# Performance work log

Hardware: AMD Instinct MI355X
Metric: run time of the kernel (lower is better)

Reference implementation:

```python
import jax, jax.numpy as jnp
import numpy as np

B, S, D, H, HID, WIN = 2, 2048, 1024, 16, 4096, 256
DH = D // H
HALF = WIN // 2  # symmetric half-window


def _layernorm(x, w, b, eps=1e-5):
    mu = jnp.mean(x, axis=-1, keepdims=True)
    var = jnp.var(x, axis=-1, keepdims=True)
    return (x - mu) * jax.lax.rsqrt(var + eps) * w + b


def setup_inputs() -> dict:
    key = jax.random.key(0)
    ks = jax.random.split(key, 8)
    std = 0.02
    return {
        "x": jax.random.normal(ks[0], (B, S, D), jnp.float32),
        "mask": jnp.ones((B, S), bool),
        "ln1_w": jnp.ones((D,), jnp.float32),
        "ln1_b": jnp.zeros((D,), jnp.float32),
        "Wq": jax.random.normal(ks[1], (D, D), jnp.float32) * std,
        "bq": jnp.zeros((D,), jnp.float32),
        "Wk": jax.random.normal(ks[2], (D, D), jnp.float32) * std,
        "bk": jnp.zeros((D,), jnp.float32),
        "Wv": jax.random.normal(ks[3], (D, D), jnp.float32) * std,
        "bv": jnp.zeros((D,), jnp.float32),
        "Wo": jax.random.normal(ks[4], (D, D), jnp.float32) * std,
        "bo": jnp.zeros((D,), jnp.float32),
        "ln2_w": jnp.ones((D,), jnp.float32),
        "ln2_b": jnp.zeros((D,), jnp.float32),
        "Wg": jax.random.normal(ks[5], (D, HID), jnp.float32) * std,
        "bg": jnp.zeros((HID,), jnp.float32),
        "Wu": jax.random.normal(ks[6], (D, HID), jnp.float32) * std,
        "bu": jnp.zeros((HID,), jnp.float32),
        "Wd": jax.random.normal(ks[7], (HID, D), jnp.float32) * std,
        "bd": jnp.zeros((D,), jnp.float32),
    }


def reference(x, mask, ln1_w, ln1_b, Wq, bq, Wk, bk, Wv, bv, Wo, bo,
              ln2_w, ln2_b, Wg, bg, Wu, bu, Wd, bd):
    # ---- pre-norm windowed self-attention ----
    h = _layernorm(x, ln1_w, ln1_b)
    q = (h @ Wq + bq).reshape(B, S, H, DH)
    k = (h @ Wk + bk).reshape(B, S, H, DH)
    v = (h @ Wv + bv).reshape(B, S, H, DH)
    scores = jnp.einsum('bshd,bthd->bhst', q, k) / jnp.sqrt(jnp.float32(DH))
    idx = jnp.arange(S)
    band = jnp.abs(idx[:, None] - idx[None, :]) <= HALF          # [S,S] sliding window
    allow = band[None, None, :, :] & mask[:, None, None, :]      # band AND key padding
    scores = jnp.where(allow, scores, jnp.float32(-1e9))
    attn = jax.nn.softmax(scores, axis=-1)
    ctx = jnp.einsum('bhst,bthd->bshd', attn, v).reshape(B, S, D)
    x = x + (ctx @ Wo + bo)
    # ---- pre-norm SwiGLU FFN ----
    h2 = _layernorm(x, ln2_w, ln2_b)
    ffn = (jax.nn.silu(h2 @ Wg + bg) * (h2 @ Wu + bu)) @ Wd + bd
    return x + ffn
```

## Files before the change

### kernel.cpp

```cpp
#include <hip/hip_runtime.h>
#include <stdint.h>


typedef __bf16 bf16;
typedef bf16  bf16x8 __attribute__((ext_vector_type(8)));
typedef bf16  bf16x4v __attribute__((ext_vector_type(4)));
typedef float f32x4  __attribute__((ext_vector_type(4)));

#define S_LEN 2048

#define GLDS16(gp, lp)                                                          \
  __builtin_amdgcn_global_load_lds(                                            \
      (__attribute__((address_space(1))) void*)(gp),                            \
      (__attribute__((address_space(3))) void*)(lp), 16, 0, 0)

__global__ __launch_bounds__(256) void ln_bf16(const float* __restrict__ x,
                                               const float* __restrict__ w,
                                               const float* __restrict__ bb,
                                               bf16* __restrict__ out) {
  const int row = blockIdx.x, tid = threadIdx.x;
  const int wid = tid >> 6, lane = tid & 63;
  const float4 v = ((const float4*)(x + (size_t)row * 1024))[tid];
  float s = v.x + v.y + v.z + v.w;
  float q = v.x * v.x + v.y * v.y + v.z * v.z + v.w * v.w;
#pragma unroll
  for (int off = 32; off > 0; off >>= 1) {
    s += __shfl_xor(s, off);
    q += __shfl_xor(q, off);
  }
  __shared__ float rs_[4], rq_[4];
  if (lane == 0) { rs_[wid] = s; rq_[wid] = q; }
  __syncthreads();
  s = rs_[0] + rs_[1] + rs_[2] + rs_[3];
  q = rq_[0] + rq_[1] + rq_[2] + rq_[3];
  const float mean = s * (1.f / 1024.f);
  const float var  = q * (1.f / 1024.f) - mean * mean;
  const float rstd = rsqrtf(var + 1e-5f);
  const float4 wv = ((const float4*)w)[tid];
  const float4 bv = ((const float4*)bb)[tid];
  bf16x4v o;
  o[0] = (bf16)((v.x - mean) * rstd * wv.x + bv.x);
  o[1] = (bf16)((v.y - mean) * rstd * wv.y + bv.y);
  o[2] = (bf16)((v.z - mean) * rstd * wv.z + bv.z);
  o[3] = (bf16)((v.w - mean) * rstd * wv.w + bv.w);
  ((bf16x4v*)(out + (size_t)row * 1024))[tid] = o;
}

__global__ __launch_bounds__(256) void tr_cast(const float* __restrict__ in,
                                               bf16* __restrict__ out, int R, int C) {
  __shared__ float t[32][33];
  const int tx = threadIdx.x, ty = threadIdx.y;
  const int r0 = blockIdx.y * 32, c0 = blockIdx.x * 32;
#pragma unroll
  for (int i = 0; i < 4; ++i)
    t[ty + 8 * i][tx] = in[(size_t)(r0 + ty + 8 * i) * C + c0 + tx];
  __syncthreads();
#pragma unroll
  for (int i = 0; i < 4; ++i)
    out[(size_t)(c0 + ty + 8 * i) * R + r0 + tx] = (bf16)t[tx][ty + 8 * i];
}

__global__ void concat3(const float* __restrict__ a, const float* __restrict__ b,
                        const float* __restrict__ c, float* __restrict__ o) {
  int i = blockIdx.x * 256 + threadIdx.x;
  if (i < 1024) o[i] = a[i];
  else if (i < 2048) o[i] = b[i - 1024];
  else if (i < 3072) o[i] = c[i - 2048];
}

#define PHASE8(p, a, b, STG, VM)                                               \
  {                                                                            \
    STG;                                                                       \
    if ((VM) == 10) asm volatile("s_waitcnt vmcnt(10)" ::: "memory");          \
    __builtin_amdgcn_s_barrier();                                              \
    const char* sA_ = smA + ((p) << 15) + ((a) << 14);                         \
    const char* sB_ = smB + ((p) << 15) + ((b) << 14);                         \
    bf16x8 av[4][2], bv[2][2];                                                 \
    _Pragma("unroll") for (int q = 0; q < 4; ++q) {                            \
      av[q][0] = *(const bf16x8*)(sA_ + aRow + q * 2048 + kh0);                \
      av[q][1] = *(const bf16x8*)(sA_ + aRow + q * 2048 + kh1);                \
    }                                                                          \
    _Pragma("unroll") for (int n_ = 0; n_ < 2; ++n_) {                         \
      bv[n_][0] = *(const bf16x8*)(sB_ + bRow + n_ * 2048 + kh0);              \
      bv[n_][1] = *(const bf16x8*)(sB_ + bRow + n_ * 2048 + kh1);              \
    }                                                                          \
    __builtin_amdgcn_s_setprio(1);                                             \
    _Pragma("unroll") for (int q = 0; q < 4; ++q)                              \
      _Pragma("unroll") for (int n_ = 0; n_ < 2; ++n_) {                       \
        acc[(a)*4 + q][(b)*2 + n_] = __builtin_amdgcn_mfma_f32_16x16x32_bf16(  \
            av[q][0], bv[n_][0], acc[(a)*4 + q][(b)*2 + n_], 0, 0, 0);         \
        acc[(a)*4 + q][(b)*2 + n_] = __builtin_amdgcn_mfma_f32_16x16x32_bf16(  \
            av[q][1], bv[n_][1], acc[(a)*4 + q][(b)*2 + n_], 0, 0, 0);         \
      }                                                                        \
    __builtin_amdgcn_s_setprio(0);                                             \
    __builtin_amdgcn_s_barrier();                                              \
  }

template <int EPI>
__global__ __launch_bounds__(512, 2) void gemm256p(
    const bf16* __restrict__ A, const bf16* __restrict__ BT,
    const bf16* __restrict__ BT2, const float* __restrict__ bias,
    const float* __restrict__ bias2, bf16* __restrict__ outp,
    bf16* __restrict__ vout, bf16* __restrict__ pout,
    int Astr, int Bstr) {
  __shared__ char smem[131072];
  char* smA = smem;
  char* smB = smem + 65536;

  const int tid = threadIdx.x, wid = tid >> 6, lane = tid & 63;
  const int fr = lane & 15, fq = lane >> 4;
  const int wr = wid >> 2, wc = wid & 3;
  const int wm = wr * 128, wn = wc * 64;

  int wg = blockIdx.x;
  {
    const int nwg = gridDim.x;
    int qq = nwg >> 3, rr = nwg & 7, xc = wg & 7, ix = wg >> 3;
    wg = (xc < rr ? xc * (qq + 1) : rr * (qq + 1) + (xc - rr) * qq) + ix;
  }
  int mtile, ntile, ks = 0;
  if constexpr (EPI == 3) { mtile = wg & 15; ntile = (wg >> 4) & 3; ks = wg >> 6; }
  else                    { mtile = wg & 15; ntile = wg >> 4; }
  const int m0 = mtile * 256;
  const int nbase = (EPI == 2) ? ntile * 128 : ntile * 256;
  const size_t kbase = (size_t)ks << 10;

  const int lr = tid >> 3;
  const int segS = ((tid & 7) ^ (lr & 7)) * 8;
  const bf16* pAc0a0 = A + (size_t)(m0 + lr) * Astr + kbase + segS;
  const bf16* pAc0a1 = A + (size_t)(m0 + 64 + lr) * Astr + kbase + segS;
  const bf16* pAc1a0 = A + (size_t)(m0 + 128 + lr) * Astr + kbase + segS;
  const bf16* pAc1a1 = A + (size_t)(m0 + 192 + lr) * Astr + kbase + segS;
  const int nn0 = (lr >> 5) * 64 + (lr & 31);
  const bf16 *pBc0b0, *pBc0b1, *pBc1b0, *pBc1b1;
  if constexpr (EPI == 2) {
    pBc0b0 = BT  + (size_t)(nbase + nn0) * Bstr + kbase + segS;
    pBc0b1 = BT  + (size_t)(nbase + nn0 + 32) * Bstr + kbase + segS;
    pBc1b0 = BT2 + (size_t)(nbase + nn0) * Bstr + kbase + segS;
    pBc1b1 = BT2 + (size_t)(nbase + nn0 + 32) * Bstr + kbase + segS;
  } else {
    pBc0b0 = BT + (size_t)(nbase + nn0) * Bstr + kbase + segS;
    pBc0b1 = BT + (size_t)(nbase + nn0 + 32) * Bstr + kbase + segS;
    pBc1b0 = BT + (size_t)(nbase + 128 + nn0) * Bstr + kbase + segS;
    pBc1b1 = BT + (size_t)(nbase + 128 + nn0 + 32) * Bstr + kbase + segS;
  }
  const int widOff = wid * 1024;

  auto stA = [&](int p, int a, int kt) {
    const size_t ko = (size_t)kt * 64;
    char* d = smA + (p << 15) + (a << 14) + widOff;
    GLDS16((a ? pAc0a1 : pAc0a0) + ko, d);
    GLDS16((a ? pAc1a1 : pAc1a0) + ko, d + 8192);
  };
  auto stB = [&](int p, int b, int kt) {
    const size_t ko = (size_t)kt * 64;
    char* d = smB + (p << 15) + (b << 14) + widOff;
    GLDS16((b ? pBc0b1 : pBc0b0) + ko, d);
    GLDS16((b ? pBc1b1 : pBc1b0) + ko, d + 8192);
  };

  const int co0 = (fq * 16) ^ ((fr & 3) << 4);
  const int kh0 = (fr & 4) << 4;
  const int kh1 = 64 ^ kh0;
  const int aRow = (wr * 64 + fr) * 128 + co0;
  const int bRow = (wc * 32 + fr) * 128 + co0;

  f32x4 acc[8][4];
#pragma unroll
  for (int i = 0; i < 8; ++i)
#pragma unroll
    for (int j = 0; j < 4; ++j) acc[i][j] = f32x4{0.f, 0.f, 0.f, 0.f};

  stB(0, 0, 0); stA(0, 0, 0); stA(0, 1, 0); stB(0, 1, 0);
  stB(1, 0, 1); stA(1, 0, 1);

  for (int t2 = 0; t2 < 8; ++t2) {
    const int te = 2 * t2, to = te + 1;
    PHASE8(0, 0, 0, stA(1, 1, (te + 1) & 15), 10)
    PHASE8(0, 1, 0, stB(1, 1, (te + 1) & 15), 10)
    PHASE8(0, 0, 1, stB(0, 0, (te + 2) & 15), 10)
    PHASE8(0, 1, 1, stA(0, 0, (te + 2) & 15), -1)
    PHASE8(1, 0, 0, stA(0, 1, (to + 1) & 15), 10)
    PHASE8(1, 1, 0, stB(0, 1, (to + 1) & 15), 10)
    PHASE8(1, 0, 1, stB(1, 0, (to + 2) & 15), 10)
    PHASE8(1, 1, 1, stA(1, 0, (to + 2) & 15), -1)
  }
  asm volatile("s_waitcnt vmcnt(0)" ::: "memory");
  __builtin_amdgcn_s_barrier();

  if constexpr (EPI == 1) {
    if (nbase < 2048) {
#pragma unroll
      for (int mi = 0; mi < 8; ++mi)
#pragma unroll
        for (int nj = 0; nj < 4; ++nj) {
          const int grow = m0 + wm + mi * 16 + fq * 4;
          const int gcol = nbase + wn + nj * 16 + fr;
          const float bc = bias[gcol];
#pragma unroll
          for (int r = 0; r < 4; ++r)
            outp[(size_t)(grow + r) * 2048 + gcol] = (bf16)(acc[mi][nj][r] + bc);
        }
    } else {
#pragma unroll
      for (int mi = 0; mi < 8; ++mi)
#pragma unroll
        for (int nj = 0; nj < 4; ++nj) {
          const int grow = m0 + wm + mi * 16 + fq * 4;
          const int gcol = nbase + wn + nj * 16 + fr;
          const float bc = bias[gcol];
          bf16x4v pk;
#pragma unroll
          for (int r = 0; r < 4; ++r) pk[r] = (bf16)(acc[mi][nj][r] + bc);
          *(bf16x4v*)(vout + ((size_t)((grow >> 11) * 1024 + (gcol - 2048))) * 2048 +
                      (grow & 2047)) = pk;
        }
    }
  } else if constexpr (EPI == 2) {
    float* uls = (float*)smem;
    if (wn >= 128) {
#pragma unroll
      for (int mi = 0; mi < 8; ++mi)
#pragma unroll
        for (int nj = 0; nj < 4; ++nj) {
          const int rowL = wm + mi * 16 + fq * 4;
          const int cu = wn - 128 + nj * 16 + fr;
          const float bc = bias2[nbase + cu];
#pragma unroll
          for (int r = 0; r < 4; ++r)
            uls[(rowL + r) * 128 + cu] = acc[mi][nj][r] + bc;
        }
    }
    __syncthreads();
    if (wn < 128) {
#pragma unroll
      for (int mi = 0; mi < 8; ++mi)
#pragma unroll
        for (int nj = 0; nj < 4; ++nj) {
          const int rowL = wm + mi * 16 + fq * 4;
          const int cg = wn + nj * 16 + fr;
          const float bc = bias[nbase + cg];
#pragma unroll
          for (int r = 0; r < 4; ++r) {
            const float g = acc[mi][nj][r] + bc;
            const float u = uls[(rowL + r) * 128 + cg];
            outp[(size_t)(m0 + rowL + r) * 4096 + nbase + cg] =
                (bf16)(g * u / (1.f + __expf(-g)));
          }
        }
    }
  } else {
    bf16* po = pout + ((size_t)ks << 22);
#pragma unroll
    for (int mi = 0; mi < 8; ++mi)
#pragma unroll
      for (int nj = 0; nj < 4; ++nj) {
        const int grow = m0 + wm + mi * 16 + fq * 4;
        const int gcol = nbase + wn + nj * 16 + fr;
#pragma unroll
        for (int r = 0; r < 4; ++r)
          po[(size_t)(grow + r) * 1024 + gcol] = (bf16)acc[mi][nj][r];
      }
  }
}

__global__ __launch_bounds__(256) void reduce_wd(
    const float* __restrict__ x1, const float* __restrict__ bd,
    const bf16* __restrict__ parts, float* __restrict__ out) {
  const size_t i = (size_t)blockIdx.x * 256 + threadIdx.x;
  const float4 a  = ((const float4*)x1)[i];
  const float4 bv = ((const float4*)bd)[i & 255];
  float s0 = a.x + bv.x, s1 = a.y + bv.y, s2 = a.z + bv.z, s3 = a.w + bv.w;
#pragma unroll
  for (int k = 0; k < 4; ++k) {
    const bf16x4v p = ((const bf16x4v*)(parts + ((size_t)k << 22)))[i];
    s0 += (float)p[0]; s1 += (float)p[1]; s2 += (float)p[2]; s3 += (float)p[3];
  }
  ((float4*)out)[i] = make_float4(s0, s1, s2, s3);
}

template <int EPI>
__global__ __launch_bounds__(256) void gemm_bf16t(
    const bf16* __restrict__ A, const bf16* __restrict__ BT,
    const float* __restrict__ bias, const float* __restrict__ res,
    void* __restrict__ Cout, int M, int N, int K) {
  __shared__ bf16 sA[128 * 64];
  __shared__ bf16 sB[128 * 64];
  const int tid = threadIdx.x;
  const int wid = tid >> 6, lane = tid & 63;
  const int m0 = blockIdx.y * 128, n0 = blockIdx.x * 128;
  const int wm = (wid >> 1) * 64, wn = (wid & 1) * 64;
  const int lrow = lane >> 3, lseg = (lane & 7) * 8;
  const int fr = lane & 15, fq = lane >> 4;

  f32x4 acc[4][4];
#pragma unroll
  for (int i = 0; i < 4; ++i)
#pragma unroll
    for (int j = 0; j < 4; ++j) acc[i][j] = f32x4{0.f, 0.f, 0.f, 0.f};

  for (int k0 = 0; k0 < K; k0 += 64) {
#pragma unroll
    for (int it = 0; it < 4; ++it) {
      const int c = wid * 4 + it;
      const int row = c * 8 + lrow;
      GLDS16(A  + (size_t)(m0 + row) * K + k0 + lseg, sA + c * 512);
      GLDS16(BT + (size_t)(n0 + row) * K + k0 + lseg, sB + c * 512);
    }
    __syncthreads();
#pragma unroll
    for (int kk = 0; kk < 64; kk += 32) {
      bf16x8 af[4], bfv[4];
#pragma unroll
      for (int i = 0; i < 4; ++i)
        af[i] = *(const bf16x8*)(sA + (wm + i * 16 + fr) * 64 + kk + 8 * fq);
#pragma unroll
      for (int j = 0; j < 4; ++j)
        bfv[j] = *(const bf16x8*)(sB + (wn + j * 16 + fr) * 64 + kk + 8 * fq);
#pragma unroll
      for (int i = 0; i < 4; ++i)
#pragma unroll
        for (int j = 0; j < 4; ++j)
          acc[i][j] = __builtin_amdgcn_mfma_f32_16x16x32_bf16(af[i], bfv[j],
                                                              acc[i][j], 0, 0, 0);
    }
    __syncthreads();
  }

#pragma unroll
  for (int i = 0; i < 4; ++i) {
    const int grow = m0 + wm + i * 16 + fq * 4;
#pragma unroll
    for (int j = 0; j < 4; ++j) {
      const int gcol = n0 + wn + j * 16 + fr;
      const float bc = bias[gcol];
#pragma unroll
      for (int r = 0; r < 4; ++r) {
        const size_t idx = (size_t)(grow + r) * N + gcol;
        const float v = acc[i][j][r] + bc;
        if constexpr (EPI == 1) {
          ((float*)Cout)[idx] = v + res[idx];
        } else {
          ((bf16*)Cout)[idx] = (bf16)v;
        }
      }
    }
  }
}

__global__ __launch_bounds__(256) void attn_mfma(const bf16* __restrict__ qk,
                                                 const bf16* __restrict__ vT,
                                                 bf16* __restrict__ ctx) {
  __shared__ bf16 sQ[64 * 72];
  __shared__ bf16 sK[320 * 72];
  __shared__ bf16 sVT[64 * 328];
  __shared__ bf16 sP[64 * 328];
  const int bh = blockIdx.x;
  const int b = bh >> 4, h = bh & 15;
  const int qs0 = blockIdx.y * 64;
  const int t0 = qs0 - 128;
  const int tS = t0 < 0 ? 0 : (t0 > S_LEN - 320 ? S_LEN - 320 : t0);
  const int tid = threadIdx.x, wid = tid >> 6, lane = tid & 63;
  const size_t bbase = (size_t)b * S_LEN;

#pragma unroll
  for (int i = 0; i < 10; ++i) {
    const int c = i * 256 + tid, row = c >> 3, seg = (c & 7) * 8;
    *(bf16x8*)(sK + row * 72 + seg) =
        *(const bf16x8*)(qk + (bbase + tS + row) * 2048 + 1024 + h * 64 + seg);
  }
#pragma unroll
  for (int i = 0; i < 2; ++i) {
    const int c = i * 256 + tid, row = c >> 3, seg = (c & 7) * 8;
    *(bf16x8*)(sQ + row * 72 + seg) =
        *(const bf16x8*)(qk + (bbase + qs0 + row) * 2048 + h * 64 + seg);
  }
  {
    const int row = tid >> 2;
    const size_t vbase = ((size_t)bh * 64 + row) * 2048 + tS;
#pragma unroll
    for (int i = 0; i < 10; ++i) {
      const int seg = ((tid & 3) + 4 * i) * 8;
      *(bf16x8*)(sVT + row * 328 + seg) = *(const bf16x8*)(vT + vbase + seg);
    }
  }
  __syncthreads();

  const int fr = lane & 15, fq = lane >> 4;

  f32x4 s[20];
#pragma unroll
  for (int j = 0; j < 20; ++j) s[j] = f32x4{0.f, 0.f, 0.f, 0.f};
#pragma unroll
  for (int kk = 0; kk < 64; kk += 32) {
    const bf16x8 aq = *(const bf16x8*)(sQ + (wid * 16 + fr) * 72 + kk + 8 * fq);
#pragma unroll
    for (int j = 0; j < 20; ++j) {
      const bf16x8 bk = *(const bf16x8*)(sK + (j * 16 + fr) * 72 + kk + 8 * fq);
      s[j] = __builtin_amdgcn_mfma_f32_16x16x32_bf16(aq, bk, s[j], 0, 0, 0);
    }
  }

#pragma unroll
  for (int r = 0; r < 4; ++r) {
    const int q_g = qs0 + wid * 16 + fq * 4 + r;
    float m = -1e30f;
#pragma unroll
    for (int j = 0; j < 20; ++j) {
      const int t_g = tS + j * 16 + fr;
      const bool ok = (unsigned)(q_g - t_g + 128) <= 256u;
      const float val = ok ? s[j][r] * 0.125f : -1e30f;
      s[j][r] = val;
      m = fmaxf(m, val);
    }
#pragma unroll
    for (int off = 1; off < 16; off <<= 1) m = fmaxf(m, __shfl_xor(m, off));
    float sm = 0.f;
#pragma unroll
    for (int j = 0; j < 20; ++j) {
      const float p = __expf(s[j][r] - m);
      s[j][r] = p;
      sm += p;
    }
#pragma unroll
    for (int off = 1; off < 16; off <<= 1) sm += __shfl_xor(sm, off);
    const float inv = 1.f / sm;
#pragma unroll
    for (int j = 0; j < 20; ++j)
      sP[(wid * 16 + fq * 4 + r) * 328 + j * 16 + fr] = (bf16)(s[j][r] * inv);
  }
  __syncthreads();

  f32x4 o[4];
#pragma unroll
  for (int j = 0; j < 4; ++j) o[j] = f32x4{0.f, 0.f, 0.f, 0.f};
#pragma unroll
  for (int ks = 0; ks < 10; ++ks) {
    const int kk = ks * 32;
    const bf16x8 pa = *(const bf16x8*)(sP + (wid * 16 + fr) * 328 + kk + 8 * fq);
#pragma unroll
    for (int j = 0; j < 4; ++j) {
      const bf16x8 vb = *(const bf16x8*)(sVT + (j * 16 + fr) * 328 + kk + 8 * fq);
      o[j] = __builtin_amdgcn_mfma_f32_16x16x32_bf16(pa, vb, o[j], 0, 0, 0);
    }
  }
#pragma unroll
  for (int j = 0; j < 4; ++j)
#pragma unroll
    for (int r = 0; r < 4; ++r) {
      const int q = qs0 + wid * 16 + fq * 4 + r;
      ctx[(bbase + q) * 1024 + h * 64 + j * 16 + fr] = (bf16)o[j][r];
    }
}

extern "C" void kernel_launch(void* const* d_in, const int* in_sizes, int n_in,
                              void* d_out, int out_size, void* d_ws, size_t ws_size,
                              hipStream_t stream) {
  const float* x    = (const float*)d_in[0];
  const float* ln1w = (const float*)d_in[2];
  const float* ln1b = (const float*)d_in[3];
  const float* Wq   = (const float*)d_in[4];
  const float* bq   = (const float*)d_in[5];
  const float* Wk   = (const float*)d_in[6];
  const float* bk   = (const float*)d_in[7];
  const float* Wv   = (const float*)d_in[8];
  const float* bv   = (const float*)d_in[9];
  const float* Wo   = (const float*)d_in[10];
  const float* bo   = (const float*)d_in[11];
  const float* ln2w = (const float*)d_in[12];
  const float* ln2b = (const float*)d_in[13];
  const float* Wg   = (const float*)d_in[14];
  const float* bg   = (const float*)d_in[15];
  const float* Wu   = (const float*)d_in[16];
  const float* bu   = (const float*)d_in[17];
  const float* Wd   = (const float*)d_in[18];
  const float* bd   = (const float*)d_in[19];

  char* ws = (char*)d_ws;
  size_t off = 0;
  auto take = [&](size_t bytes) {
    char* p = ws + off;
    off += (bytes + 255) & ~(size_t)255;
    return p;
  };
  bf16*  wqkvT = (bf16*)take((size_t)3072 * 1024 * 2);
  bf16*  woT   = (bf16*)take((size_t)1024 * 1024 * 2);
  bf16*  wgT   = (bf16*)take((size_t)4096 * 1024 * 2);
  bf16*  wuT   = (bf16*)take((size_t)4096 * 1024 * 2);
  bf16*  wdT   = (bf16*)take((size_t)1024 * 4096 * 2);
  float* bqkv  = (float*)take((size_t)3072 * 4);
  bf16*  h     = (bf16*)take((size_t)4096 * 1024 * 2);
  bf16*  qk    = (bf16*)take((size_t)4096 * 2048 * 2);
  bf16*  ctx   = (bf16*)take((size_t)4096 * 1024 * 2);
  bf16*  vT    = (bf16*)take((size_t)2048 * 2048 * 2);
  float* x1    = (float*)take((size_t)4096 * 1024 * 4);
  bf16*  h2    = (bf16*)take((size_t)4096 * 1024 * 2);
  bf16*  gated = (bf16*)take((size_t)4096 * 4096 * 2);
  bf16*  parts = h;
  (void)ws_size; (void)in_sizes; (void)n_in; (void)out_size;

  const dim3 tb(32, 8);
  tr_cast<<<dim3(32, 32), tb, 0, stream>>>(Wq, wqkvT, 1024, 1024);
  tr_cast<<<dim3(32, 32), tb, 0, stream>>>(Wk, wqkvT + (size_t)1024 * 1024, 1024, 1024);
  tr_cast<<<dim3(32, 32), tb, 0, stream>>>(Wv, wqkvT + (size_t)2048 * 1024, 1024, 1024);
  tr_cast<<<dim3(32, 32), tb, 0, stream>>>(Wo, woT, 1024, 1024);
  tr_cast<<<dim3(128, 32), tb, 0, stream>>>(Wg, wgT, 1024, 4096);
  tr_cast<<<dim3(128, 32), tb, 0, stream>>>(Wu, wuT, 1024, 4096);
  tr_cast<<<dim3(32, 128), tb, 0, stream>>>(Wd, wdT, 4096, 1024);
  concat3<<<12, 256, 0, stream>>>(bq, bk, bv, bqkv);

  ln_bf16<<<4096, 256, 0, stream>>>(x, ln1w, ln1b, h);
  gemm256p<1><<<192, 512, 0, stream>>>(h, wqkvT, nullptr, bqkv, nullptr,
                                       qk, vT, nullptr, 1024, 1024);
  attn_mfma<<<dim3(32, 32), 256, 0, stream>>>(qk, vT, ctx);
  gemm_bf16t<1><<<dim3(8, 32), 256, 0, stream>>>(ctx, woT, bo, x,
                                                 x1, 4096, 1024, 1024);
  ln_bf16<<<4096, 256, 0, stream>>>(x1, ln2w, ln2b, h2);
  gemm256p<2><<<512, 512, 0, stream>>>(h2, wgT, wuT, bg, bu, gated,
                                       nullptr, nullptr, 1024, 1024);
  gemm256p<3><<<256, 512, 0, stream>>>(gated, wdT, nullptr, nullptr, nullptr,
                                       nullptr, nullptr, parts, 4096, 4096);
  reduce_wd<<<4096, 256, 0, stream>>>(x1, bd, parts, (float*)d_out);
}
```

Baseline: 265.8 us.

## Replace 8-phase GEMM pipeline with simple double-buffered stage/compute loop

Replaces the fine-grained 8-phase interleaved staging schedule (quarter-tile loads and barriers per phase) with a plain two-buffer ping-pong. Each full k-tile of A and B is loaded into one buffer while the other is computed. Each wave now loads a contiguous 32-row slab, and each warp covers its whole 128x64 output per compute step, reusing B fragments across two A halves. This cuts barrier count and scheduling complexity, but gives coarser overlap of global loads with MFMA work.

```diff
diff --git a/kernel.cpp b/kernel.cpp
--- a/kernel.cpp
+++ b/kernel.cpp
@@ -68,34 +68,6 @@
   else if (i < 3072) o[i] = c[i - 2048];
 }
 
-#define PHASE8(p, a, b, STG, VM)                                               \
-  {                                                                            \
-    STG;                                                                       \
-    if ((VM) == 10) asm volatile("s_waitcnt vmcnt(10)" ::: "memory");          \
-    __builtin_amdgcn_s_barrier();                                              \
-    const char* sA_ = smA + ((p) << 15) + ((a) << 14);                         \
-    const char* sB_ = smB + ((p) << 15) + ((b) << 14);                         \
-    bf16x8 av[4][2], bv[2][2];                                                 \
-    _Pragma("unroll") for (int q = 0; q < 4; ++q) {                            \
-      av[q][0] = *(const bf16x8*)(sA_ + aRow + q * 2048 + kh0);                \
-      av[q][1] = *(const bf16x8*)(sA_ + aRow + q * 2048 + kh1);                \
-    }                                                                          \
-    _Pragma("unroll") for (int n_ = 0; n_ < 2; ++n_) {                         \
-      bv[n_][0] = *(const bf16x8*)(sB_ + bRow + n_ * 2048 + kh0);              \
-      bv[n_][1] = *(const bf16x8*)(sB_ + bRow + n_ * 2048 + kh1);              \
-    }                                                                          \
-    __builtin_amdgcn_s_setprio(1);                                             \
-    _Pragma("unroll") for (int q = 0; q < 4; ++q)                              \
-      _Pragma("unroll") for (int n_ = 0; n_ < 2; ++n_) {                       \
-        acc[(a)*4 + q][(b)*2 + n_] = __builtin_amdgcn_mfma_f32_16x16x32_bf16(  \
-            av[q][0], bv[n_][0], acc[(a)*4 + q][(b)*2 + n_], 0, 0, 0);         \
-        acc[(a)*4 + q][(b)*2 + n_] = __builtin_amdgcn_mfma_f32_16x16x32_bf16(  \
-            av[q][1], bv[n_][1], acc[(a)*4 + q][(b)*2 + n_], 0, 0, 0);         \
-      }                                                                        \
-    __builtin_amdgcn_s_setprio(0);                                             \
-    __builtin_amdgcn_s_barrier();                                              \
-  }
-
 template <int EPI>
 __global__ __launch_bounds__(512, 2) void gemm256p(
     const bf16* __restrict__ A, const bf16* __restrict__ BT,
@@ -104,8 +76,10 @@
     bf16* __restrict__ vout, bf16* __restrict__ pout,
     int Astr, int Bstr) {
   __shared__ char smem[131072];
-  char* smA = smem;
-  char* smB = smem + 65536;
+  char* A0 = smem;
+  char* A1 = smem + 32768;
+  char* B0 = smem + 65536;
+  char* B1 = smem + 98304;
 
   const int tid = threadIdx.x, wid = tid >> 6, lane = tid & 63;
   const int fr = lane & 15, fq = lane >> 4;
@@ -125,45 +99,34 @@
   const int nbase = (EPI == 2) ? ntile * 128 : ntile * 256;
   const size_t kbase = (size_t)ks << 10;
 
-  const int lr = tid >> 3;
-  const int segS = ((tid & 7) ^ (lr & 7)) * 8;
-  const bf16* pAc0a0 = A + (size_t)(m0 + lr) * Astr + kbase + segS;
-  const bf16* pAc0a1 = A + (size_t)(m0 + 64 + lr) * Astr + kbase + segS;
-  const bf16* pAc1a0 = A + (size_t)(m0 + 128 + lr) * Astr + kbase + segS;
-  const bf16* pAc1a1 = A + (size_t)(m0 + 192 + lr) * Astr + kbase + segS;
-  const int nn0 = (lr >> 5) * 64 + (lr & 31);
-  const bf16 *pBc0b0, *pBc0b1, *pBc1b0, *pBc1b1;
+  const int srow = lane >> 3;
+  const int segS = ((lane & 7) ^ srow) * 8;
+  const size_t rsA8 = (size_t)8 * Astr;
+  const size_t rsB8 = (size_t)8 * Bstr;
+  const bf16* pA = A + (size_t)(m0 + wid * 32 + srow) * Astr + kbase + segS;
+  const bf16* pB;
   if constexpr (EPI == 2) {
-    pBc0b0 = BT  + (size_t)(nbase + nn0) * Bstr + kbase + segS;
-    pBc0b1 = BT  + (size_t)(nbase + nn0 + 32) * Bstr + kbase + segS;
-    pBc1b0 = BT2 + (size_t)(nbase + nn0) * Bstr + kbase + segS;
-    pBc1b1 = BT2 + (size_t)(nbase + nn0 + 32) * Bstr + kbase + segS;
+    const bf16* srcB = (wid < 4) ? BT : BT2;
+    pB = srcB + (size_t)(nbase + (wid & 3) * 32 + srow) * Bstr + kbase + segS;
   } else {
-    pBc0b0 = BT + (size_t)(nbase + nn0) * Bstr + kbase + segS;
-    pBc0b1 = BT + (size_t)(nbase + nn0 + 32) * Bstr + kbase + segS;
-    pBc1b0 = BT + (size_t)(nbase + 128 + nn0) * Bstr + kbase + segS;
-    pBc1b1 = BT + (size_t)(nbase + 128 + nn0 + 32) * Bstr + kbase + segS;
-  }
-  const int widOff = wid * 1024;
-
-  auto stA = [&](int p, int a, int kt) {
+    pB = BT + (size_t)(nbase + wid * 32 + srow) * Bstr + kbase + segS;
+  }
+  const int cOff = wid * 4096;
+
+  auto STAGE = [&](char* aD, char* bD, int kt) {
     const size_t ko = (size_t)kt * 64;
-    char* d = smA + (p << 15) + (a << 14) + widOff;
-    GLDS16((a ? pAc0a1 : pAc0a0) + ko, d);
-    GLDS16((a ? pAc1a1 : pAc1a0) + ko, d + 8192);
-  };
-  auto stB = [&](int p, int b, int kt) {
-    const size_t ko = (size_t)kt * 64;
-    char* d = smB + (p << 15) + (b << 14) + widOff;
-    GLDS16((b ? pBc0b1 : pBc0b0) + ko, d);
-    GLDS16((b ? pBc1b1 : pBc1b0) + ko, d + 8192);
+#pragma unroll
+    for (int i = 0; i < 4; ++i) {
+      GLDS16(pA + i * rsA8 + ko, aD + cOff + i * 1024);
+      GLDS16(pB + i * rsB8 + ko, bD + cOff + i * 1024);
+    }
   };
 
   const int co0 = (fq * 16) ^ ((fr & 3) << 4);
   const int kh0 = (fr & 4) << 4;
   const int kh1 = 64 ^ kh0;
-  const int aRow = (wr * 64 + fr) * 128 + co0;
-  const int bRow = (wc * 32 + fr) * 128 + co0;
+  const int aOff = (wm + fr) * 128 + co0;
+  const int bOff = (wn + fr) * 128 + co0;
 
   f32x4 acc[8][4];
 #pragma unroll
@@ -171,22 +134,55 @@
 #pragma unroll
     for (int j = 0; j < 4; ++j) acc[i][j] = f32x4{0.f, 0.f, 0.f, 0.f};
 
-  stB(0, 0, 0); stA(0, 0, 0); stA(0, 1, 0); stB(0, 1, 0);
-  stB(1, 0, 1); stA(1, 0, 1);
-
-  for (int t2 = 0; t2 < 8; ++t2) {
-    const int te = 2 * t2, to = te + 1;
-    PHASE8(0, 0, 0, stA(1, 1, (te + 1) & 15), 10)
-    PHASE8(0, 1, 0, stB(1, 1, (te + 1) & 15), 10)
-    PHASE8(0, 0, 1, stB(0, 0, (te + 2) & 15), 10)
-    PHASE8(0, 1, 1, stA(0, 0, (te + 2) & 15), -1)
-    PHASE8(1, 0, 0, stA(0, 1, (to + 1) & 15), 10)
-    PHASE8(1, 1, 0, stB(0, 1, (to + 1) & 15), 10)
-    PHASE8(1, 0, 1, stB(1, 0, (to + 2) & 15), 10)
-    PHASE8(1, 1, 1, stA(1, 0, (to + 2) & 15), -1)
-  }
-  asm volatile("s_waitcnt vmcnt(0)" ::: "memory");
-  __builtin_amdgcn_s_barrier();
+  auto COMPUTE = [&](const char* aB, const char* bB) {
+#pragma unroll
+    for (int kh = 0; kh < 2; ++kh) {
+      const int khX = kh ? kh1 : kh0;
+      bf16x8 bv[4], av[4];
+#pragma unroll
+      for (int nj = 0; nj < 4; ++nj)
+        bv[nj] = *(const bf16x8*)(bB + bOff + nj * 2048 + khX);
+#pragma unroll
+      for (int q = 0; q < 4; ++q)
+        av[q] = *(const bf16x8*)(aB + aOff + q * 2048 + khX);
+      __builtin_amdgcn_s_setprio(1);
+#pragma unroll
+      for (int q = 0; q < 4; ++q)
+#pragma unroll
+        for (int nj = 0; nj < 4; ++nj)
+          acc[q][nj] = __builtin_amdgcn_mfma_f32_16x16x32_bf16(
+              av[q], bv[nj], acc[q][nj], 0, 0, 0);
+      __builtin_amdgcn_s_setprio(0);
+#pragma unroll
+      for (int q = 0; q < 4; ++q)
+        av[q] = *(const bf16x8*)(aB + aOff + 8192 + q * 2048 + khX);
+      __builtin_amdgcn_s_setprio(1);
+#pragma unroll
+      for (int q = 0; q < 4; ++q)
+#pragma unroll
+        for (int nj = 0; nj < 4; ++nj)
+          acc[4 + q][nj] = __builtin_amdgcn_mfma_f32_16x16x32_bf16(
+              av[q], bv[nj], acc[4 + q][nj], 0, 0, 0);
+      __builtin_amdgcn_s_setprio(0);
+    }
+  };
+
+#define VM8()  asm volatile("s_waitcnt vmcnt(8)" ::: "memory")
+#define VM0()  asm volatile("s_waitcnt vmcnt(0)" ::: "memory")
+#define BAR()  __builtin_amdgcn_s_barrier()
+
+  STAGE(A0, B0, 0);
+#pragma unroll 1
+  for (int t2 = 0; t2 < 7; ++t2) {
+    STAGE(A1, B1, 2 * t2 + 1);  VM8();  BAR();
+    COMPUTE(A0, B0);            BAR();
+    STAGE(A0, B0, 2 * t2 + 2);  VM8();  BAR();
+    COMPUTE(A1, B1);            BAR();
+  }
+  STAGE(A1, B1, 15);  VM8();  BAR();
+  COMPUTE(A0, B0);    BAR();
+  VM0();  BAR();
+  COMPUTE(A1, B1);    BAR();
 
   if constexpr (EPI == 1) {
     if (nbase < 2048) {
@@ -262,6 +258,9 @@
           po[(size_t)(grow + r) * 1024 + gcol] = (bf16)acc[mi][nj][r];
       }
   }
+#undef VM8
+#undef VM0
+#undef BAR
 }
 
 __global__ __launch_bounds__(256) void reduce_wd(
```

Result: no change. 262.9 us (-1.1%).
